# Kernel tuning notes

Measured on AMD Instinct MI355X. Metric: run time of the kernel, lower is better.

The kernel has to match this reference:

```python
import jax, jax.numpy as jnp
import numpy as np

N_NODES = 50000
N_EDGES = 800000
NFEAT = 128
NHID = 64  # gc1: NFEAT -> 2*NHID, gc2: 2*NHID -> NHID


def setup_inputs() -> dict:
    key = jax.random.key(0)
    k1, k2, k3, k4, k5 = jax.random.split(key, 5)
    feat = jax.random.normal(k1, (N_NODES, NFEAT), dtype=jnp.float32)
    src = jax.random.randint(k2, (N_EDGES,), 0, N_NODES, dtype=jnp.int32)
    dst = jax.random.randint(k3, (N_EDGES,), 0, N_NODES, dtype=jnp.int32)
    # GraphConv weights: (in_feats, out_feats), xavier-like scale
    W1 = jax.random.normal(k4, (NFEAT, 2 * NHID), dtype=jnp.float32) / np.sqrt(NFEAT)
    b1 = jnp.zeros((2 * NHID,), dtype=jnp.float32)
    W2 = jax.random.normal(k5, (2 * NHID, NHID), dtype=jnp.float32) / np.sqrt(2 * NHID)
    b2 = jnp.zeros((NHID,), dtype=jnp.float32)
    return {"feat": feat, "src": src, "dst": dst, "W1": W1, "b1": b1, "W2": W2, "b2": b2}


def _graph_conv(feat, src, dst, W, b):
    """DGL GraphConv, norm='both', allow_zero_in_degree=True.
    h = D_in^{-1/2} A (D_out^{-1/2} x) W + b, with degrees clamped to >= 1.
    Applies W before aggregation when in_feats > out_feats (saves bandwidth)."""
    N = feat.shape[0]
    ones = jnp.ones(src.shape[0], dtype=feat.dtype)
    deg_out = jnp.clip(jax.ops.segment_sum(ones, src, num_segments=N), 1.0)
    deg_in = jnp.clip(jax.ops.segment_sum(ones, dst, num_segments=N), 1.0)
    h = feat * (deg_out ** -0.5)[:, None]
    mult_first = W.shape[0] > W.shape[1]
    if mult_first:
        h = h @ W
    agg = jax.ops.segment_sum(h[src], dst, num_segments=N)  # [N, d]
    if not mult_first:
        agg = agg @ W
    return agg * (deg_in ** -0.5)[:, None] + b


def reference(feat, src, dst, W1, b1, W2, b2):
    x = jax.nn.relu(_graph_conv(feat, src, dst, W1, b1))
    # dropout is inactive in eval mode (F.dropout training=False)
    x = _graph_conv(x, src, dst, W2, b2)
    return jax.nn.log_softmax(x, axis=1)
```

## Files before the change

kernel.cpp:

```cpp
#include <hip/hip_runtime.h>
#include <math.h>


constexpr int NF   = 128;
constexpr int NH   = 64;
constexpr int CAP  = 48;
constexpr int EPB  = 4096;
constexpr int BCAP = 8192;
constexpr int NBKMAX = 256;
constexpr int FWB  = 180;

typedef unsigned int uint;
typedef unsigned short ushort_t;
typedef __attribute__((ext_vector_type(8))) short short8;
typedef __attribute__((ext_vector_type(4))) float f32x4;

__device__ __forceinline__ float bflo(uint u) { return __uint_as_float(u << 16); }
__device__ __forceinline__ float bfhi(uint u) { return __uint_as_float(u & 0xffff0000u); }
__device__ __forceinline__ uint packbf(float a, float b) {
    uint ua = __float_as_uint(a), ub = __float_as_uint(b);
    uint ra = (ua + 0x7fffu + ((ua >> 16) & 1u)) >> 16;
    uint rb = (ub + 0x7fffu + ((ub >> 16) & 1u)) >> 16;
    return ra | (rb << 16);
}
__device__ __forceinline__ ushort_t bf16u(float f) {
    uint u = __float_as_uint(f);
    return (ushort_t)((u + 0x7fffu + ((u >> 16) & 1u)) >> 16);
}
__device__ __forceinline__ short8 as_short8(uint4 u) {
    union { uint4 u; short8 s; } x; x.u = u; return x.s;
}

__global__ __launch_bounds__(1024) void prep_kernel(
        const float* __restrict__ W1, const float* __restrict__ W2,
        uint* __restrict__ W1p, uint* __restrict__ W2p,
        int* __restrict__ dcur, int* __restrict__ scur, int nbk) {
    int i = blockIdx.x * 1024 + threadIdx.x;
    if (i < 8192) {
        int jp = i & 3, g = (i >> 2) & 3, n = (i >> 4) & 127, kk = i >> 11;
        int k = kk * 32 + g * 8 + jp * 2;
        W1p[i] = packbf(W1[k * 128 + n], W1[(k + 1) * 128 + n]);
    } else if (i < 12288) {
        int j = i - 8192;
        int jp = j & 3, g = (j >> 2) & 3, n = (j >> 4) & 63, kk = j >> 10;
        int k = kk * 32 + g * 8 + jp * 2;
        W2p[j] = packbf(W2[k * 64 + n], W2[(k + 1) * 64 + n]);
    } else {
        int z = i - 12288;
        if (z < nbk) dcur[z] = 0;
        else if (z < 2 * nbk) scur[z - nbk] = 0;
    }
}

__global__ __launch_bounds__(1024) void partition_kernel(
        const int* __restrict__ src, const int* __restrict__ dst,
        uint* __restrict__ pairs_g, ushort_t* __restrict__ srcb_g,
        int* __restrict__ dcur, int* __restrict__ scur,
        const uint* __restrict__ W1p,
        const float* __restrict__ feat, uint* __restrict__ featW,
        int E, int nbk, int nchunk, int N) {
    if (blockIdx.x >= nchunk) {
        __shared__ ushort_t xt[64][136];
        int xb = blockIdx.x - nchunk;
        int tid = threadIdx.x;
        int w = tid >> 6, lane = tid & 63, c = lane & 15, g = lane >> 4;
        int mt = w & 3, np = w >> 2;
        int sr = tid >> 4, f0 = (tid & 15) * 8;
        int ntile = (N + 63) >> 6;
        f32x4 zero = {0.f, 0.f, 0.f, 0.f};
        for (int tile = xb; tile < ntile; tile += FWB) {
            int tb = tile << 6;
            {
                int row = tb + sr;
                uint4 o = make_uint4(0, 0, 0, 0);
                if (row < N) {
                    const float4* f4 = (const float4*)(feat + (size_t)row * NF + f0);
                    float4 a = f4[0], cc = f4[1];
                    o.x = packbf(a.x, a.y);  o.y = packbf(a.z, a.w);
                    o.z = packbf(cc.x, cc.y); o.w = packbf(cc.z, cc.w);
                }
                *(uint4*)&xt[sr][f0] = o;
            }
            __syncthreads();
            f32x4 c1[2]; c1[0] = zero; c1[1] = zero;
            #pragma unroll
            for (int kk = 0; kk < 4; ++kk) {
                short8 af = *(const short8*)&xt[mt * 16 + c][kk * 32 + g * 8];
                #pragma unroll
                for (int ntl = 0; ntl < 2; ++ntl) {
                    int n = (np * 2 + ntl) * 16 + c;
                    short8 bf = as_short8(*(const uint4*)(W1p + (size_t)kk * 2048 + n * 16 + g * 4));
                    c1[ntl] = __builtin_amdgcn_mfma_f32_16x16x32_bf16(af, bf, c1[ntl], 0, 0, 0);
                }
            }
            __syncthreads();
            #pragma unroll
            for (int ntl = 0; ntl < 2; ++ntl) {
                #pragma unroll
                for (int rr = 0; rr < 4; ++rr)
                    xt[mt * 16 + g * 4 + rr][(np * 2 + ntl) * 16 + c] = bf16u(c1[ntl][rr]);
            }
            __syncthreads();
            {
                int row = tid >> 4, u0 = (tid & 15) * 4;
                if (tb + row < N)
                    *(uint4*)(featW + (size_t)(tb + row) * 64 + u0) =
                        *(const uint4*)((const uint*)&xt[0][0] + row * 68 + u0);
            }
            __syncthreads();
        }
        return;
    }
    __shared__ uint     pl[EPB];
    __shared__ ushort_t sl[EPB];
    __shared__ int dh[NBKMAX], sh[NBKMAX];
    __shared__ int doff[NBKMAX], soff[NBKMAX];
    __shared__ int dbase[NBKMAX], sbase[NBKMAX];
    __shared__ int dpos[NBKMAX], spos[NBKMAX];
    int tid = threadIdx.x;
    int e0 = blockIdx.x * EPB;
    int ecnt = min(EPB, E - e0);
    int ecnt4 = ecnt >> 2;
    bool own = tid < ecnt4;
    int4 sR = make_int4(0, 0, 0, 0), dR = make_int4(0, 0, 0, 0);
    if (own) {
        sR = ((const int4*)(src + e0))[tid];
        dR = ((const int4*)(dst + e0))[tid];
    }

    for (int b = tid; b < nbk; b += 1024) { dh[b] = 0; sh[b] = 0; }
    __syncthreads();
    if (own) {
        atomicAdd(&dh[dR.x >> 8], 1); atomicAdd(&dh[dR.y >> 8], 1);
        atomicAdd(&dh[dR.z >> 8], 1); atomicAdd(&dh[dR.w >> 8], 1);
        atomicAdd(&sh[sR.x >> 8], 1); atomicAdd(&sh[sR.y >> 8], 1);
        atomicAdd(&sh[sR.z >> 8], 1); atomicAdd(&sh[sR.w >> 8], 1);
    }
    for (int i = ecnt4 * 4 + tid; i < ecnt; i += 1024) {
        atomicAdd(&dh[dst[e0 + i] >> 8], 1);
        atomicAdd(&sh[src[e0 + i] >> 8], 1);
    }
    __syncthreads();
    if (tid < 128) {
        int wv = tid >> 6, l = tid & 63, b0 = l * 4;
        const int* h = wv ? sh : dh;
        int* of      = wv ? soff : doff;
        int v0 = (b0     < nbk) ? h[b0]     : 0;
        int v1 = (b0 + 1 < nbk) ? h[b0 + 1] : 0;
        int v2 = (b0 + 2 < nbk) ? h[b0 + 2] : 0;
        int v3 = (b0 + 3 < nbk) ? h[b0 + 3] : 0;
        int lsum = v0 + v1 + v2 + v3;
        int sc = lsum;
        #pragma unroll
        for (int off = 1; off < 64; off <<= 1) {
            int t = __shfl_up(sc, off, 64);
            if (l >= off) sc += t;
        }
        int excl = sc - lsum;
        if (b0     < nbk) of[b0]     = excl;
        if (b0 + 1 < nbk) of[b0 + 1] = excl + v0;
        if (b0 + 2 < nbk) of[b0 + 2] = excl + v0 + v1;
        if (b0 + 3 < nbk) of[b0 + 3] = excl + v0 + v1 + v2;
    }
    for (int b = tid; b < nbk; b += 1024) {
        dbase[b] = atomicAdd(&dcur[b], dh[b]);
        sbase[b] = atomicAdd(&scur[b], sh[b]);
    }
    __syncthreads();
    for (int b = tid; b < nbk; b += 1024) { dpos[b] = doff[b]; spos[b] = soff[b]; }
    __syncthreads();
    if (own) {
        #pragma unroll
        for (int j = 0; j < 4; ++j) {
            int sj = (j == 0) ? sR.x : (j == 1) ? sR.y : (j == 2) ? sR.z : sR.w;
            int dj = (j == 0) ? dR.x : (j == 1) ? dR.y : (j == 2) ? dR.z : dR.w;
            int p = atomicAdd(&dpos[dj >> 8], 1);
            pl[p] = ((uint)sj << 16) | (uint)dj;
            int q = atomicAdd(&spos[sj >> 8], 1);
            sl[q] = (ushort_t)sj;
        }
    }
    for (int i = ecnt4 * 4 + tid; i < ecnt; i += 1024) {
        int s = src[e0 + i], d = dst[e0 + i];
        int p = atomicAdd(&dpos[d >> 8], 1);
        pl[p] = ((uint)s << 16) | (uint)d;
        int q = atomicAdd(&spos[s >> 8], 1);
        sl[q] = (ushort_t)s;
    }
    __syncthreads();
    if (own) {
        uint4 e4 = *(const uint4*)&pl[tid * 4];
        ushort4 s4 = *(const ushort4*)&sl[tid * 4];
        #pragma unroll
        for (int j = 0; j < 4; ++j) {
            uint e = (j == 0) ? e4.x : (j == 1) ? e4.y : (j == 2) ? e4.z : e4.w;
            int i = tid * 4 + j;
            int b = (int)((e & 0xffffu) >> 8);
            int gp = dbase[b] + (i - doff[b]);
            if (gp < BCAP) pairs_g[(size_t)b * BCAP + gp] = e;
            ushort_t sv = (j == 0) ? s4.x : (j == 1) ? s4.y : (j == 2) ? s4.z : s4.w;
            int b2 = (int)(sv >> 8);
            int gq = sbase[b2] + (i - soff[b2]);
            if (gq < BCAP) srcb_g[(size_t)b2 * BCAP + gq] = sv;
        }
    }
    for (int i = ecnt4 * 4 + tid; i < ecnt; i += 1024) {
        uint e = pl[i];
        int b = (int)((e & 0xffffu) >> 8);
        int gp = dbase[b] + (i - doff[b]);
        if (gp < BCAP) pairs_g[(size_t)b * BCAP + gp] = e;
        ushort_t sv = sl[i];
        int b2 = (int)(sv >> 8);
        int gq = sbase[b2] + (i - soff[b2]);
        if (gq < BCAP) srcb_g[(size_t)b2 * BCAP + gq] = sv;
    }
}

__global__ __launch_bounds__(1024) void bin_kernel(
        const uint* __restrict__ pairs_g, const ushort_t* __restrict__ srcb_g,
        const int* __restrict__ dcur, const int* __restrict__ scur,
        ushort_t* __restrict__ slots, int* __restrict__ lens,
        float* __restrict__ s_in, float* __restrict__ s_out, int N) {
    __shared__ ushort_t slots_l[256 * CAP];
    __shared__ int cin[256], cout[256];
    int tid = threadIdx.x;
    int b = blockIdx.x;
    int lo = b << 8;
    for (int r = tid; r < 256; r += 1024) { cin[r] = 0; cout[r] = 0; }
    __syncthreads();
    int dn = min(dcur[b], BCAP);
    for (int i = tid; i < dn; i += 1024) {
        uint e = pairs_g[(size_t)b * BCAP + i];
        int r = (int)(e & 255u);
        int p = atomicAdd(&cin[r], 1);
        if (p < CAP) slots_l[r * CAP + p] = (ushort_t)(e >> 16);
    }
    int sn = min(scur[b], BCAP);
    for (int i = tid; i < sn; i += 1024)
        atomicAdd(&cout[(int)srcb_g[(size_t)b * BCAP + i] - lo], 1);
    __syncthreads();
    int nrow = min(256, N - lo);
    {
        const uint4* sl4 = (const uint4*)slots_l;
        uint4* gs4 = (uint4*)(slots + (size_t)lo * CAP);
        int lim4 = nrow * (CAP / 8);
        for (int k = tid; k < 256 * CAP / 8; k += 1024)
            if (k < lim4) gs4[k] = sl4[k];
    }
    for (int r = tid; r < nrow; r += 1024) {
        int node = lo + r;
        int ci = cin[r];
        lens[node]  = min(ci, CAP);
        s_in[node]  = rsqrtf((float)max(ci, 1));
        s_out[node] = rsqrtf((float)max(cout[r], 1));
    }
}

__global__ __launch_bounds__(1024) void agg1_fused_kernel(
        const uint* __restrict__ featW,
        const int* __restrict__ lens, const ushort_t* __restrict__ slots,
        const float* __restrict__ s_in, const float* __restrict__ s_out,
        const float* __restrict__ b1, const uint* __restrict__ W2p,
        uint* __restrict__ h2b, int N) {
    __shared__ ushort_t x1t[16][136];
    __shared__ ushort_t h2t[16][72];
    int tid  = threadIdx.x;
    int wv   = tid >> 6;
    int lane = tid & 63;
    int q    = lane >> 4;
    int sub  = lane & 15;
    int base = blockIdx.x * 16;
    int node = base + wv;

    float acc[8] = {0.f, 0.f, 0.f, 0.f, 0.f, 0.f, 0.f, 0.f};
    if (node < N) {
        int beg = node * CAP;
        int len = lens[node];
        if (len > 0) {
            int li = min(lane, len - 1);
            int sidx = (int)slots[beg + li];
            int quads = (len + 3) >> 2;
            #pragma unroll 4
            for (int k = 0; k < quads; ++k) {
                int e = 4 * k + q;
                int s = __shfl(sidx, e, 64);
                if (e < len) {
                    float so = s_out[s];
                    uint4 v = *(const uint4*)(featW + (size_t)s * 64 + sub * 4);
                    acc[0] = fmaf(so, bflo(v.x), acc[0]);
                    acc[1] = fmaf(so, bfhi(v.x), acc[1]);
                    acc[2] = fmaf(so, bflo(v.y), acc[2]);
                    acc[3] = fmaf(so, bfhi(v.y), acc[3]);
                    acc[4] = fmaf(so, bflo(v.z), acc[4]);
                    acc[5] = fmaf(so, bfhi(v.z), acc[5]);
                    acc[6] = fmaf(so, bflo(v.w), acc[6]);
                    acc[7] = fmaf(so, bfhi(v.w), acc[7]);
                }
            }
        }
        #pragma unroll
        for (int j = 0; j < 8; ++j) {
            acc[j] += __shfl_xor(acc[j], 32, 64);
            acc[j] += __shfl_xor(acc[j], 16, 64);
        }
        if (q == 0) {
            float si = s_in[node], so = s_out[node];
            float4 bb0 = *(const float4*)(b1 + sub * 8);
            float4 bb1 = *(const float4*)(b1 + sub * 8 + 4);
            float x0 = fmaxf(fmaf(si, acc[0], bb0.x), 0.f) * so;
            float x1 = fmaxf(fmaf(si, acc[1], bb0.y), 0.f) * so;
            float x2 = fmaxf(fmaf(si, acc[2], bb0.z), 0.f) * so;
            float x3 = fmaxf(fmaf(si, acc[3], bb0.w), 0.f) * so;
            float x4 = fmaxf(fmaf(si, acc[4], bb1.x), 0.f) * so;
            float x5 = fmaxf(fmaf(si, acc[5], bb1.y), 0.f) * so;
            float x6 = fmaxf(fmaf(si, acc[6], bb1.z), 0.f) * so;
            float x7 = fmaxf(fmaf(si, acc[7], bb1.w), 0.f) * so;
            uint4 o;
            o.x = packbf(x0, x1); o.y = packbf(x2, x3);
            o.z = packbf(x4, x5); o.w = packbf(x6, x7);
            *(uint4*)&x1t[wv][sub * 8] = o;
        }
    } else if (q == 0) {
        uint4 z = make_uint4(0, 0, 0, 0);
        *(uint4*)&x1t[wv][sub * 8] = z;
    }
    __syncthreads();

    if (wv < 4) {
        f32x4 c2 = {0.f, 0.f, 0.f, 0.f};
        int n = wv * 16 + sub;
        #pragma unroll
        for (int kk = 0; kk < 4; ++kk) {
            short8 bf2 = as_short8(*(const uint4*)(W2p + (size_t)kk * 1024 + n * 16 + q * 4));
            short8 af = *(const short8*)&x1t[sub][kk * 32 + q * 8];
            c2 = __builtin_amdgcn_mfma_f32_16x16x32_bf16(af, bf2, c2, 0, 0, 0);
        }
        #pragma unroll
        for (int r = 0; r < 4; ++r)
            h2t[q * 4 + r][wv * 16 + sub] = bf16u(c2[r]);
    }
    __syncthreads();

    if (tid < 128) {
        int row = tid >> 3, u0 = (tid & 7) * 4;
        if (base + row < N)
            *(uint4*)(h2b + (size_t)(base + row) * 32 + u0) =
                *(const uint4*)((const uint*)&h2t[row][0] + u0);
    }
}

__global__ __launch_bounds__(256) void agg2_softmax_kernel(const uint* __restrict__ h2b,
        const int* __restrict__ lens, const ushort_t* __restrict__ slots,
        const float* __restrict__ s_in, const float* __restrict__ b2,
        float* __restrict__ out, int N) {
    int wave = threadIdx.x >> 6;
    int lane = threadIdx.x & 63;
    int oct = lane >> 3;
    int sub = lane & 7;
    int node = blockIdx.x * 4 + wave;
    if (node >= N) return;
    int beg = node * CAP;
    int len = lens[node];
    float acc[8] = {0.f, 0.f, 0.f, 0.f, 0.f, 0.f, 0.f, 0.f};
    if (len > 0) {
        int li = min(lane, len - 1);
        int sidx = (int)slots[beg + li];
        int octs = (len + 7) >> 3;
        #pragma unroll 4
        for (int k = 0; k < octs; ++k) {
            int e = 8 * k + oct;
            int s = __shfl(sidx, e, 64);
            if (e < len) {
                uint4 v = *(const uint4*)(h2b + (size_t)s * 32 + sub * 4);
                acc[0] += bflo(v.x); acc[1] += bfhi(v.x);
                acc[2] += bflo(v.y); acc[3] += bfhi(v.y);
                acc[4] += bflo(v.z); acc[5] += bfhi(v.z);
                acc[6] += bflo(v.w); acc[7] += bfhi(v.w);
            }
        }
    }
    #pragma unroll
    for (int j = 0; j < 8; ++j) {
        acc[j] += __shfl_xor(acc[j], 32, 64);
        acc[j] += __shfl_xor(acc[j], 16, 64);
        acc[j] += __shfl_xor(acc[j], 8, 64);
    }
    float si = s_in[node];
    float4 bb0 = *(const float4*)(b2 + sub * 8);
    float4 bb1 = *(const float4*)(b2 + sub * 8 + 4);
    float v[8];
    v[0] = fmaf(acc[0], si, bb0.x); v[1] = fmaf(acc[1], si, bb0.y);
    v[2] = fmaf(acc[2], si, bb0.z); v[3] = fmaf(acc[3], si, bb0.w);
    v[4] = fmaf(acc[4], si, bb1.x); v[5] = fmaf(acc[5], si, bb1.y);
    v[6] = fmaf(acc[6], si, bb1.z); v[7] = fmaf(acc[7], si, bb1.w);

    float m = v[0];
    #pragma unroll
    for (int j = 1; j < 8; ++j) m = fmaxf(m, v[j]);
    m = fmaxf(m, __shfl_xor(m, 4, 64));
    m = fmaxf(m, __shfl_xor(m, 2, 64));
    m = fmaxf(m, __shfl_xor(m, 1, 64));
    float s8 = 0.f;
    #pragma unroll
    for (int j = 0; j < 8; ++j) s8 += expf(v[j] - m);
    s8 += __shfl_xor(s8, 4, 64);
    s8 += __shfl_xor(s8, 2, 64);
    s8 += __shfl_xor(s8, 1, 64);
    float ls = m + logf(s8);
    if (oct == 0) {
        float4 o0 = make_float4(v[0] - ls, v[1] - ls, v[2] - ls, v[3] - ls);
        float4 o1 = make_float4(v[4] - ls, v[5] - ls, v[6] - ls, v[7] - ls);
        *(float4*)(out + (size_t)node * NH + sub * 8)     = o0;
        *(float4*)(out + (size_t)node * NH + sub * 8 + 4) = o1;
    }
}

extern "C" void kernel_launch(void* const* d_in, const int* in_sizes, int n_in,
                              void* d_out, int out_size, void* d_ws, size_t ws_size,
                              hipStream_t stream) {
    const float* feat = (const float*)d_in[0];
    const int*   src  = (const int*)d_in[1];
    const int*   dst  = (const int*)d_in[2];
    const float* W1   = (const float*)d_in[3];
    const float* b1   = (const float*)d_in[4];
    const float* W2   = (const float*)d_in[5];
    const float* b2   = (const float*)d_in[6];
    float* out = (float*)d_out;

    int N = in_sizes[0] / NF;
    int E = in_sizes[1];
    int nbk = (N + 255) >> 8;
    int nchunk = (E + EPB - 1) / EPB;

    char* p = (char*)d_ws;
    auto alloc = [&](size_t bytes) -> char* {
        char* q = p;
        p += (bytes + 255) & ~(size_t)255;
        return q;
    };
    int*      dcur  = (int*)alloc((size_t)nbk * 4);
    int*      scur  = (int*)alloc((size_t)nbk * 4);
    uint*     pairs = (uint*)alloc((size_t)nbk * BCAP * 4);
    ushort_t* srcb  = (ushort_t*)alloc((size_t)nbk * BCAP * 2);
    ushort_t* slots = (ushort_t*)alloc((size_t)N * CAP * 2);
    int*      lens  = (int*)alloc((size_t)N * 4);
    float*    s_out = (float*)alloc((size_t)N * 4);
    float*    s_in  = (float*)alloc((size_t)N * 4);
    uint*     featW = (uint*)alloc((size_t)N * 64 * 4);
    uint*     W1p   = (uint*)alloc(8192 * 4);
    uint*     W2p   = (uint*)alloc(4096 * 4);
    uint*     h2b   = (uint*)alloc((size_t)N * 32 * 4);

    prep_kernel<<<13, 1024, 0, stream>>>(W1, W2, W1p, W2p, dcur, scur, nbk);
    partition_kernel<<<nchunk + FWB, 1024, 0, stream>>>(
        src, dst, pairs, srcb, dcur, scur, W1p, feat, featW, E, nbk, nchunk, N);
    bin_kernel<<<nbk, 1024, 0, stream>>>(pairs, srcb, dcur, scur,
                                         slots, lens, s_in, s_out, N);
    agg1_fused_kernel<<<(N + 15) / 16, 1024, 0, stream>>>(
        featW, lens, slots, s_in, s_out, b1, W2p, h2b, N);
    agg2_softmax_kernel<<<(N + 3) / 4, 256, 0, stream>>>(h2b, lens, slots, s_in, b2, out, N);
}
```

Before: 169.9 us.

## Remove prep kernel, move weight packing and feature GEMM to other stages

Drops the separate prep kernel. Weight packing now runs in extra blocks of the partition kernel, and the counter zeroing becomes a hipMemsetAsync. The feature×W1 bf16 GEMM blocks move from the partition kernel into the bin kernel, so partition no longer waits on packed weights and the GEMM overlaps binning instead. This saves one launch and fixes a dependency, but the bin kernel's larger shared-memory use in the GEMM blocks may change its occupancy.

Result: no change. 171.1 us (+0.7%).

```diff
diff --git a/kernel.cpp b/kernel.cpp
--- a/kernel.cpp
+++ b/kernel.cpp
@@ -31,37 +31,142 @@
     union { uint4 u; short8 s; } x; x.u = u; return x.s;
 }
 
-__global__ __launch_bounds__(1024) void prep_kernel(
-        const float* __restrict__ W1, const float* __restrict__ W2,
-        uint* __restrict__ W1p, uint* __restrict__ W2p,
-        int* __restrict__ dcur, int* __restrict__ scur, int nbk) {
-    int i = blockIdx.x * 1024 + threadIdx.x;
-    if (i < 8192) {
-        int jp = i & 3, g = (i >> 2) & 3, n = (i >> 4) & 127, kk = i >> 11;
-        int k = kk * 32 + g * 8 + jp * 2;
-        W1p[i] = packbf(W1[k * 128 + n], W1[(k + 1) * 128 + n]);
-    } else if (i < 12288) {
-        int j = i - 8192;
-        int jp = j & 3, g = (j >> 2) & 3, n = (j >> 4) & 63, kk = j >> 10;
-        int k = kk * 32 + g * 8 + jp * 2;
-        W2p[j] = packbf(W2[k * 64 + n], W2[(k + 1) * 64 + n]);
-    } else {
-        int z = i - 12288;
-        if (z < nbk) dcur[z] = 0;
-        else if (z < 2 * nbk) scur[z - nbk] = 0;
-    }
-}
-
 __global__ __launch_bounds__(1024) void partition_kernel(
         const int* __restrict__ src, const int* __restrict__ dst,
         uint* __restrict__ pairs_g, ushort_t* __restrict__ srcb_g,
         int* __restrict__ dcur, int* __restrict__ scur,
-        const uint* __restrict__ W1p,
-        const float* __restrict__ feat, uint* __restrict__ featW,
-        int E, int nbk, int nchunk, int N) {
+        const float* __restrict__ W1, const float* __restrict__ W2,
+        uint* __restrict__ W1p, uint* __restrict__ W2p,
+        int E, int nbk, int nchunk) {
     if (blockIdx.x >= nchunk) {
+        int i = (blockIdx.x - nchunk) * 1024 + threadIdx.x;
+        if (i < 8192) {
+            int jp = i & 3, g = (i >> 2) & 3, n = (i >> 4) & 127, kk = i >> 11;
+            int k = kk * 32 + g * 8 + jp * 2;
+            W1p[i] = packbf(W1[k * 128 + n], W1[(k + 1) * 128 + n]);
+        } else if (i < 12288) {
+            int j = i - 8192;
+            int jp = j & 3, g = (j >> 2) & 3, n = (j >> 4) & 63, kk = j >> 10;
+            int k = kk * 32 + g * 8 + jp * 2;
+            W2p[j] = packbf(W2[k * 64 + n], W2[(k + 1) * 64 + n]);
+        }
+        return;
+    }
+    __shared__ uint     pl[EPB];
+    __shared__ ushort_t sl[EPB];
+    __shared__ int dh[NBKMAX], sh[NBKMAX];
+    __shared__ int doff[NBKMAX], soff[NBKMAX];
+    __shared__ int dbase[NBKMAX], sbase[NBKMAX];
+    __shared__ int dpos[NBKMAX], spos[NBKMAX];
+    int tid = threadIdx.x;
+    int e0 = blockIdx.x * EPB;
+    int ecnt = min(EPB, E - e0);
+    int ecnt4 = ecnt >> 2;
+    bool own = tid < ecnt4;
+    int4 sR = make_int4(0, 0, 0, 0), dR = make_int4(0, 0, 0, 0);
+    if (own) {
+        sR = ((const int4*)(src + e0))[tid];
+        dR = ((const int4*)(dst + e0))[tid];
+    }
+
+    for (int b = tid; b < nbk; b += 1024) { dh[b] = 0; sh[b] = 0; }
+    __syncthreads();
+    if (own) {
+        atomicAdd(&dh[dR.x >> 8], 1); atomicAdd(&dh[dR.y >> 8], 1);
+        atomicAdd(&dh[dR.z >> 8], 1); atomicAdd(&dh[dR.w >> 8], 1);
+        atomicAdd(&sh[sR.x >> 8], 1); atomicAdd(&sh[sR.y >> 8], 1);
+        atomicAdd(&sh[sR.z >> 8], 1); atomicAdd(&sh[sR.w >> 8], 1);
+    }
+    for (int i = ecnt4 * 4 + tid; i < ecnt; i += 1024) {
+        atomicAdd(&dh[dst[e0 + i] >> 8], 1);
+        atomicAdd(&sh[src[e0 + i] >> 8], 1);
+    }
+    __syncthreads();
+    if (tid < 128) {
+        int wv = tid >> 6, l = tid & 63, b0 = l * 4;
+        const int* h = wv ? sh : dh;
+        int* of      = wv ? soff : doff;
+        int v0 = (b0     < nbk) ? h[b0]     : 0;
+        int v1 = (b0 + 1 < nbk) ? h[b0 + 1] : 0;
+        int v2 = (b0 + 2 < nbk) ? h[b0 + 2] : 0;
+        int v3 = (b0 + 3 < nbk) ? h[b0 + 3] : 0;
+        int lsum = v0 + v1 + v2 + v3;
+        int sc = lsum;
+        #pragma unroll
+        for (int off = 1; off < 64; off <<= 1) {
+            int t = __shfl_up(sc, off, 64);
+            if (l >= off) sc += t;
+        }
+        int excl = sc - lsum;
+        if (b0     < nbk) of[b0]     = excl;
+        if (b0 + 1 < nbk) of[b0 + 1] = excl + v0;
+        if (b0 + 2 < nbk) of[b0 + 2] = excl + v0 + v1;
+        if (b0 + 3 < nbk) of[b0 + 3] = excl + v0 + v1 + v2;
+    }
+    for (int b = tid; b < nbk; b += 1024) {
+        dbase[b] = atomicAdd(&dcur[b], dh[b]);
+        sbase[b] = atomicAdd(&scur[b], sh[b]);
+    }
+    __syncthreads();
+    for (int b = tid; b < nbk; b += 1024) { dpos[b] = doff[b]; spos[b] = soff[b]; }
+    __syncthreads();
+    if (own) {
+        #pragma unroll
+        for (int j = 0; j < 4; ++j) {
+            int sj = (j == 0) ? sR.x : (j == 1) ? sR.y : (j == 2) ? sR.z : sR.w;
+            int dj = (j == 0) ? dR.x : (j == 1) ? dR.y : (j == 2) ? dR.z : dR.w;
+            int p = atomicAdd(&dpos[dj >> 8], 1);
+            pl[p] = ((uint)sj << 16) | (uint)dj;
+            int q = atomicAdd(&spos[sj >> 8], 1);
+            sl[q] = (ushort_t)sj;
+        }
+    }
+    for (int i = ecnt4 * 4 + tid; i < ecnt; i += 1024) {
+        int s = src[e0 + i], d = dst[e0 + i];
+        int p = atomicAdd(&dpos[d >> 8], 1);
+        pl[p] = ((uint)s << 16) | (uint)d;
+        int q = atomicAdd(&spos[s >> 8], 1);
+        sl[q] = (ushort_t)s;
+    }
+    __syncthreads();
+    if (own) {
+        uint4 e4 = *(const uint4*)&pl[tid * 4];
+        ushort4 s4 = *(const ushort4*)&sl[tid * 4];
+        #pragma unroll
+        for (int j = 0; j < 4; ++j) {
+            uint e = (j == 0) ? e4.x : (j == 1) ? e4.y : (j == 2) ? e4.z : e4.w;
+            int i = tid * 4 + j;
+            int b = (int)((e & 0xffffu) >> 8);
+            int gp = dbase[b] + (i - doff[b]);
+            if (gp < BCAP) pairs_g[(size_t)b * BCAP + gp] = e;
+            ushort_t sv = (j == 0) ? s4.x : (j == 1) ? s4.y : (j == 2) ? s4.z : s4.w;
+            int b2 = (int)(sv >> 8);
+            int gq = sbase[b2] + (i - soff[b2]);
+            if (gq < BCAP) srcb_g[(size_t)b2 * BCAP + gq] = sv;
+        }
+    }
+    for (int i = ecnt4 * 4 + tid; i < ecnt; i += 1024) {
+        uint e = pl[i];
+        int b = (int)((e & 0xffffu) >> 8);
+        int gp = dbase[b] + (i - doff[b]);
+        if (gp < BCAP) pairs_g[(size_t)b * BCAP + gp] = e;
+        ushort_t sv = sl[i];
+        int b2 = (int)(sv >> 8);
+        int gq = sbase[b2] + (i - soff[b2]);
+        if (gq < BCAP) srcb_g[(size_t)b2 * BCAP + gq] = sv;
+    }
+}
+
+__global__ __launch_bounds__(1024) void bin_kernel(
+        const uint* __restrict__ pairs_g, const ushort_t* __restrict__ srcb_g,
+        const int* __restrict__ dcur, const int* __restrict__ scur,
+        ushort_t* __restrict__ slots, int* __restrict__ lens,
+        float* __restrict__ s_in, float* __restrict__ s_out,
+        const uint* __restrict__ W1p, const float* __restrict__ feat,
+        uint* __restrict__ featW, int nbk, int N) {
+    if (blockIdx.x >= nbk) {
         __shared__ ushort_t xt[64][136];
-        int xb = blockIdx.x - nchunk;
+        int xb = blockIdx.x - nbk;
         int tid = threadIdx.x;
         int w = tid >> 6, lane = tid & 63, c = lane & 15, g = lane >> 4;
         int mt = w & 3, np = w >> 2;
@@ -111,116 +216,6 @@
         }
         return;
     }
-    __shared__ uint     pl[EPB];
-    __shared__ ushort_t sl[EPB];
-    __shared__ int dh[NBKMAX], sh[NBKMAX];
-    __shared__ int doff[NBKMAX], soff[NBKMAX];
-    __shared__ int dbase[NBKMAX], sbase[NBKMAX];
-    __shared__ int dpos[NBKMAX], spos[NBKMAX];
-    int tid = threadIdx.x;
-    int e0 = blockIdx.x * EPB;
-    int ecnt = min(EPB, E - e0);
-    int ecnt4 = ecnt >> 2;
-    bool own = tid < ecnt4;
-    int4 sR = make_int4(0, 0, 0, 0), dR = make_int4(0, 0, 0, 0);
-    if (own) {
-        sR = ((const int4*)(src + e0))[tid];
-        dR = ((const int4*)(dst + e0))[tid];
-    }
-
-    for (int b = tid; b < nbk; b += 1024) { dh[b] = 0; sh[b] = 0; }
-    __syncthreads();
-    if (own) {
-        atomicAdd(&dh[dR.x >> 8], 1); atomicAdd(&dh[dR.y >> 8], 1);
-        atomicAdd(&dh[dR.z >> 8], 1); atomicAdd(&dh[dR.w >> 8], 1);
-        atomicAdd(&sh[sR.x >> 8], 1); atomicAdd(&sh[sR.y >> 8], 1);
-        atomicAdd(&sh[sR.z >> 8], 1); atomicAdd(&sh[sR.w >> 8], 1);
-    }
-    for (int i = ecnt4 * 4 + tid; i < ecnt; i += 1024) {
-        atomicAdd(&dh[dst[e0 + i] >> 8], 1);
-        atomicAdd(&sh[src[e0 + i] >> 8], 1);
-    }
-    __syncthreads();
-    if (tid < 128) {
-        int wv = tid >> 6, l = tid & 63, b0 = l * 4;
-        const int* h = wv ? sh : dh;
-        int* of      = wv ? soff : doff;
-        int v0 = (b0     < nbk) ? h[b0]     : 0;
-        int v1 = (b0 + 1 < nbk) ? h[b0 + 1] : 0;
-        int v2 = (b0 + 2 < nbk) ? h[b0 + 2] : 0;
-        int v3 = (b0 + 3 < nbk) ? h[b0 + 3] : 0;
-        int lsum = v0 + v1 + v2 + v3;
-        int sc = lsum;
-        #pragma unroll
-        for (int off = 1; off < 64; off <<= 1) {
-            int t = __shfl_up(sc, off, 64);
-            if (l >= off) sc += t;
-        }
-        int excl = sc - lsum;
-        if (b0     < nbk) of[b0]     = excl;
-        if (b0 + 1 < nbk) of[b0 + 1] = excl + v0;
-        if (b0 + 2 < nbk) of[b0 + 2] = excl + v0 + v1;
-        if (b0 + 3 < nbk) of[b0 + 3] = excl + v0 + v1 + v2;
-    }
-    for (int b = tid; b < nbk; b += 1024) {
-        dbase[b] = atomicAdd(&dcur[b], dh[b]);
-        sbase[b] = atomicAdd(&scur[b], sh[b]);
-    }
-    __syncthreads();
-    for (int b = tid; b < nbk; b += 1024) { dpos[b] = doff[b]; spos[b] = soff[b]; }
-    __syncthreads();
-    if (own) {
-        #pragma unroll
-        for (int j = 0; j < 4; ++j) {
-            int sj = (j == 0) ? sR.x : (j == 1) ? sR.y : (j == 2) ? sR.z : sR.w;
-            int dj = (j == 0) ? dR.x : (j == 1) ? dR.y : (j == 2) ? dR.z : dR.w;
-            int p = atomicAdd(&dpos[dj >> 8], 1);
-            pl[p] = ((uint)sj << 16) | (uint)dj;
-            int q = atomicAdd(&spos[sj >> 8], 1);
-            sl[q] = (ushort_t)sj;
-        }
-    }
-    for (int i = ecnt4 * 4 + tid; i < ecnt; i += 1024) {
-        int s = src[e0 + i], d = dst[e0 + i];
-        int p = atomicAdd(&dpos[d >> 8], 1);
-        pl[p] = ((uint)s << 16) | (uint)d;
-        int q = atomicAdd(&spos[s >> 8], 1);
-        sl[q] = (ushort_t)s;
-    }
-    __syncthreads();
-    if (own) {
-        uint4 e4 = *(const uint4*)&pl[tid * 4];
-        ushort4 s4 = *(const ushort4*)&sl[tid * 4];
-        #pragma unroll
-        for (int j = 0; j < 4; ++j) {
-            uint e = (j == 0) ? e4.x : (j == 1) ? e4.y : (j == 2) ? e4.z : e4.w;
-            int i = tid * 4 + j;
-            int b = (int)((e & 0xffffu) >> 8);
-            int gp = dbase[b] + (i - doff[b]);
-            if (gp < BCAP) pairs_g[(size_t)b * BCAP + gp] = e;
-            ushort_t sv = (j == 0) ? s4.x : (j == 1) ? s4.y : (j == 2) ? s4.z : s4.w;
-            int b2 = (int)(sv >> 8);
-            int gq = sbase[b2] + (i - soff[b2]);
-            if (gq < BCAP) srcb_g[(size_t)b2 * BCAP + gq] = sv;
-        }
-    }
-    for (int i = ecnt4 * 4 + tid; i < ecnt; i += 1024) {
-        uint e = pl[i];
-        int b = (int)((e & 0xffffu) >> 8);
-        int gp = dbase[b] + (i - doff[b]);
-        if (gp < BCAP) pairs_g[(size_t)b * BCAP + gp] = e;
-        ushort_t sv = sl[i];
-        int b2 = (int)(sv >> 8);
-        int gq = sbase[b2] + (i - soff[b2]);
-        if (gq < BCAP) srcb_g[(size_t)b2 * BCAP + gq] = sv;
-    }
-}
-
-__global__ __launch_bounds__(1024) void bin_kernel(
-        const uint* __restrict__ pairs_g, const ushort_t* __restrict__ srcb_g,
-        const int* __restrict__ dcur, const int* __restrict__ scur,
-        ushort_t* __restrict__ slots, int* __restrict__ lens,
-        float* __restrict__ s_in, float* __restrict__ s_out, int N) {
     __shared__ ushort_t slots_l[256 * CAP];
     __shared__ int cin[256], cout[256];
     int tid = threadIdx.x;
@@ -451,11 +446,14 @@
     uint*     W2p   = (uint*)alloc(4096 * 4);
     uint*     h2b   = (uint*)alloc((size_t)N * 32 * 4);
 
-    prep_kernel<<<13, 1024, 0, stream>>>(W1, W2, W1p, W2p, dcur, scur, nbk);
-    partition_kernel<<<nchunk + FWB, 1024, 0, stream>>>(
-        src, dst, pairs, srcb, dcur, scur, W1p, feat, featW, E, nbk, nchunk, N);
-    bin_kernel<<<nbk, 1024, 0, stream>>>(pairs, srcb, dcur, scur,
-                                         slots, lens, s_in, s_out, N);
+    size_t cur_span = (size_t)((char*)scur - (char*)dcur) + (size_t)nbk * 4;
+    hipMemsetAsync(dcur, 0, cur_span, stream);
+
+    partition_kernel<<<nchunk + 12, 1024, 0, stream>>>(
+        src, dst, pairs, srcb, dcur, scur, W1, W2, W1p, W2p, E, nbk, nchunk);
+    bin_kernel<<<nbk + FWB, 1024, 0, stream>>>(pairs, srcb, dcur, scur,
+                                               slots, lens, s_in, s_out,
+                                               W1p, feat, featW, nbk, N);
     agg1_fused_kernel<<<(N + 15) / 16, 1024, 0, stream>>>(
         featW, lens, slots, s_in, s_out, b1, W2p, h2b, N);
     agg2_softmax_kernel<<<(N + 3) / 4, 256, 0, stream>>>(h2b, lens, slots, s_in, b2, out, N);
```
